# Optimization experiments

Hardware: AMD Instinct MI355X
Metric: run time of the kernel (lower is better)

The kernel has to match this reference:

```python
import jax, jax.numpy as jnp
import numpy as np

LSH_NUM_PROJS = 7
BLOCK_SIZE = 256      # key block size
SAMPLE_SIZE = 256
B, H, N, D = 1, 32, 8192, 128


def _gray_perm(num_projs):
    # AngularLSH._unit_hamming_distance_array: Gray-code bucket permutation
    a = np.array([0, 1], dtype=np.int32)
    for _ in range(num_projs - 1):
        a = np.concatenate([a, np.flip(a) + a.shape[0]])
    return jnp.asarray(a)


def _lsh_hash(x, proj_dir, perm):
    # x: [B,H,N,D], proj_dir: [D,R] -> bucket ids [B,H,N]
    bits = jnp.einsum('bhnd,dr->bhnr', x, proj_dir) > 0
    enc = 2 ** jnp.arange(proj_dir.shape[-1], dtype=jnp.int32)
    bin_ids = jnp.sum(bits.astype(jnp.int32) * enc, axis=-1)
    return perm[bin_ids]


def _attn_lse(q, k, v, scale, bias=None):
    # exact attention returning output and log-sum-exp of scaled scores
    s = jnp.einsum('...qd,...kd->...qk', q, k) * scale
    if bias is not None:
        s = s + bias
    m = jnp.max(s, axis=-1, keepdims=True)
    p = jnp.exp(s - m)
    denom = jnp.sum(p, axis=-1, keepdims=True)
    attn = jnp.einsum('...qk,...kd->...qd', p, v) / denom
    lse = m + jnp.log(denom)  # [..., q, 1]
    return attn, lse


def _take(x, idx):
    # gather along the sequence axis (dim 2); idx: [B,H,M]
    return jnp.take_along_axis(x, idx[..., None], axis=2)


def hyper_attention(q, k, v, proj_dir, sampled_set):
    b, h, n, d = q.shape
    scale = d ** -0.5
    perm = _gray_perm(LSH_NUM_PROJS)
    # 1) sortLSH: sort q and k by angular-LSH bucket (stable)
    q_idx = jnp.argsort(_lsh_hash(q, proj_dir, perm), axis=2)
    k_idx = jnp.argsort(_lsh_hash(k, proj_dir, perm), axis=2)
    q_idx_inv = jnp.argsort(q_idx, axis=2)
    q_s = _take(q, q_idx)
    k_s = _take(k, k_idx)
    v_s = _take(v, k_idx)
    nb = n // BLOCK_SIZE          # number of key blocks
    qbs = n // nb                 # query block size
    # block-diagonal exact attention in sorted order
    qb = q_s.reshape(b, h, nb, qbs, d)
    kb = k_s.reshape(b, h, nb, BLOCK_SIZE, d)
    vb = v_s.reshape(b, h, nb, BLOCK_SIZE, d)
    attn_blk, lse_blk = _attn_lse(qb, kb, vb, scale)
    attn_blk = attn_blk.reshape(b, h, n, d)
    lse_blk = lse_blk.reshape(b, h, n, 1)
    attn_blk = _take(attn_blk, q_idx_inv)
    lse_blk = _take(lse_blk, q_idx_inv)
    # 2) residual: uniform sampling of keys (indices into sorted key order)
    s_size = sampled_set.shape[-1]
    k_sub = _take(k_s, sampled_set)   # [B,H,S,D]
    v_sub = _take(v_s, sampled_set)
    # mask out samples falling in the query's own diagonal block
    same_block = (jnp.arange(n)[None, None, :, None] // qbs) == (sampled_set[:, :, None, :] // BLOCK_SIZE)
    bias = jnp.where(same_block, jnp.finfo(q.dtype).min, 0.0).astype(q.dtype)
    attn_res, lse_res = _attn_lse(q_s, k_sub, v_sub, scale, bias=bias)
    lse_res = lse_res + jnp.log(n / s_size)  # importance weight n_key/sample_size
    attn_res = _take(attn_res, q_idx_inv)
    lse_res = _take(lse_res, q_idx_inv)
    # 3) combine estimators: softmax-weighted average in log space
    lse = jnp.logaddexp(lse_blk, lse_res)
    return jnp.exp(lse_blk - lse) * attn_blk + jnp.exp(lse_res - lse) * attn_res


def setup_inputs() -> dict:
    key = jax.random.key(0)
    k1, k2, k3, k4, k5 = jax.random.split(key, 5)
    return {
        'queries': jax.random.normal(k1, (B, H, N, D), dtype=jnp.float32),
        'keys': jax.random.normal(k2, (B, H, N, D), dtype=jnp.float32),
        'vals': jax.random.normal(k3, (B, H, N, D), dtype=jnp.float32),
        'proj_dir': jax.random.normal(k4, (D, LSH_NUM_PROJS), dtype=jnp.float32),
        'sampled_set': jax.random.randint(k5, (B, H, SAMPLE_SIZE), 0, N),
    }


def reference(queries, keys, vals, proj_dir, sampled_set):
    return hyper_attention(queries, keys, vals, proj_dir, sampled_set)
```

## Files before the change

### kernel.cpp

```cpp
#include <hip/hip_runtime.h>
#include <hip/hip_bf16.h>
#include <math.h>

#define Hh 32
#define Nseq 8192
#define Dh 128
#define NBd 32
#define BLKSZ 256
#define SAMP 256
#define KVT 512
#define CHK 64
#define NCH 8
#define LOG32 3.4657359027997265f
#define SCALE 0.088388347648318447f
#define SKW 136

typedef float f32x4 __attribute__((ext_vector_type(4)));
typedef unsigned ui32x4 __attribute__((ext_vector_type(4)));
typedef __bf16 bf16x8 __attribute__((ext_vector_type(8)));

__device__ __forceinline__ f32x4 mfma16(bf16x8 a, bf16x8 b, f32x4 c) {
  return __builtin_amdgcn_mfma_f32_16x16x32_bf16(a, b, c, 0, 0, 0);
}

__device__ __forceinline__ bf16x8 cvt8(const float* __restrict__ p) {
  float4 a = ((const float4*)p)[0];
  float4 b = ((const float4*)p)[1];
  bf16x8 r;
  r[0] = (__bf16)a.x; r[1] = (__bf16)a.y; r[2] = (__bf16)a.z; r[3] = (__bf16)a.w;
  r[4] = (__bf16)b.x; r[5] = (__bf16)b.y; r[6] = (__bf16)b.z; r[7] = (__bf16)b.w;
  return r;
}

__device__ __forceinline__ bf16x8 cvt8v(float4 a, float4 b) {
  bf16x8 r;
  r[0] = (__bf16)a.x; r[1] = (__bf16)a.y; r[2] = (__bf16)a.z; r[3] = (__bf16)a.w;
  r[4] = (__bf16)b.x; r[5] = (__bf16)b.y; r[6] = (__bf16)b.z; r[7] = (__bf16)b.w;
  return r;
}

__device__ __forceinline__ unsigned packv(float a, float b) {
  __bf16 ba = (__bf16)a, bb = (__bf16)b;
  return ((unsigned)__builtin_bit_cast(unsigned short, bb) << 16) |
         (unsigned)__builtin_bit_cast(unsigned short, ba);
}

__device__ __forceinline__ unsigned pack2(float a, float b, float& ra, float& rb) {
  __bf16 ba = (__bf16)a, bb = (__bf16)b;
  ra = (float)ba; rb = (float)bb;
  return ((unsigned)__builtin_bit_cast(unsigned short, bb) << 16) |
         (unsigned)__builtin_bit_cast(unsigned short, ba);
}

__global__ __launch_bounds__(256) void lsh_hash_kernel(
    const float* __restrict__ q, const float* __restrict__ k,
    const float* __restrict__ proj, int* __restrict__ buckets) {
  int row = blockIdx.x * 256 + threadIdx.x;
  const float* x = ((row >> 18) ? k : q) + (size_t)(row & (Hh * Nseq - 1)) * Dh;
  double acc[7] = {0, 0, 0, 0, 0, 0, 0};
#pragma unroll 8
  for (int d0 = 0; d0 < Dh; d0 += 4) {
    float4 xv = *(const float4*)(x + d0);
    double x0 = (double)xv.x, x1 = (double)xv.y, x2 = (double)xv.z, x3 = (double)xv.w;
#pragma unroll
    for (int j = 0; j < 7; j++) {
      acc[j] = fma(x0, (double)proj[(d0 + 0) * 7 + j], acc[j]);
      acc[j] = fma(x1, (double)proj[(d0 + 1) * 7 + j], acc[j]);
      acc[j] = fma(x2, (double)proj[(d0 + 2) * 7 + j], acc[j]);
      acc[j] = fma(x3, (double)proj[(d0 + 3) * 7 + j], acc[j]);
    }
  }
  int bin = 0;
#pragma unroll
  for (int j = 0; j < 7; j++) bin |= (acc[j] > 0.0 ? 1 : 0) << j;
  buckets[row] = bin ^ (bin >> 1);
}

__global__ __launch_bounds__(64) void bucket_sort_kernel(
    const int* __restrict__ buckets, int* __restrict__ idx) {
  __shared__ unsigned hist[64][128];
  int t = threadIdx.x;
  int base = blockIdx.x * Nseq;
  for (int b = 0; b < 128; b++) hist[t][b] = 0;
  __syncthreads();
  for (int i = 0; i < 128; i++) {
    int b = buckets[base + t * 128 + i];
    hist[t][b]++;
  }
  __syncthreads();
  int b0 = 2 * t, b1 = 2 * t + 1;
  unsigned tot0 = 0, tot1 = 0;
  for (int tt = 0; tt < 64; tt++) { unsigned h = hist[tt][b0]; hist[tt][b0] = tot0; tot0 += h; }
  for (int tt = 0; tt < 64; tt++) { unsigned h = hist[tt][b1]; hist[tt][b1] = tot1; tot1 += h; }
  unsigned pair = tot0 + tot1;
  unsigned scan = pair;
  for (int s = 1; s < 64; s <<= 1) {
    unsigned u = __shfl_up(scan, s);
    if (t >= s) scan += u;
  }
  unsigned start0 = scan - pair;
  unsigned start1 = start0 + tot0;
  __syncthreads();
  for (int tt = 0; tt < 64; tt++) { hist[tt][b0] += start0; hist[tt][b1] += start1; }
  __syncthreads();
  for (int i = 0; i < 128; i++) {
    int gi = t * 128 + i;
    int b = buckets[base + gi];
    unsigned pos = hist[t][b]++;
    idx[base + pos] = gi;
  }
}

__global__ __launch_bounds__(512, 2) void hyper_attn_kernel(
    const float* __restrict__ q, const float* __restrict__ k, const float* __restrict__ v,
    const int* __restrict__ sampled, const int* __restrict__ q_idx,
    const int* __restrict__ k_idx, float* __restrict__ out) {
  __shared__ int s_orig[KVT];
  __shared__ __attribute__((aligned(16))) float s_add[KVT];
  __shared__ __attribute__((aligned(16))) __bf16 s_k[2][CHK][SKW];
  __shared__ __attribute__((aligned(16))) __bf16 s_vt[2][Dh][72];

  const int swz = ((blockIdx.x & 7) << 7) | (blockIdx.x >> 3);
  const int c = swz & 31, bh = swz >> 5;
  const int tid = threadIdx.x;
  const int w = tid >> 6, l = tid & 63;
  const int l4 = l >> 4, lm = l & 15;
  const int jk = tid >> 3, pk = tid & 7;
  const int kb = (tid & 31) * 2, dg = tid >> 5;

  {
    int jj = tid;
    if (jj < BLKSZ) {
      s_orig[jj] = k_idx[bh * Nseq + c * BLKSZ + jj];
      s_add[jj] = 0.0f;
    } else {
      int sp = sampled[bh * SAMP + (jj - BLKSZ)];
      s_orig[jj] = k_idx[bh * Nseq + sp];
      s_add[jj] = ((sp >> 8) == c) ? -1e38f : LOG32;
    }
  }

  bf16x8 qf[2][4];
  const int* qi = q_idx + bh * Nseq + c * BLKSZ + w * 32;
#pragma unroll
  for (int rt = 0; rt < 2; rt++) {
    int orig = qi[rt * 16 + lm];
    const float* qp = q + ((size_t)bh * Nseq + orig) * Dh + l4 * 8;
#pragma unroll
    for (int dc = 0; dc < 4; dc++) qf[rt][dc] = cvt8(qp + dc * 32);
  }

  f32x4 O[2][8];
  float mrow[2] = {-INFINITY, -INFINITY};
  float lsum[2] = {0.f, 0.f};
#pragma unroll
  for (int rt = 0; rt < 2; rt++)
#pragma unroll
    for (int dt = 0; dt < 8; dt++) { O[rt][dt][0]=0.f; O[rt][dt][1]=0.f; O[rt][dt][2]=0.f; O[rt][dt][3]=0.f; }

  __syncthreads();

  {
    int origk = s_orig[jk];
    const float* kp = k + ((size_t)bh * Nseq + origk) * Dh + pk * 16;
    *(bf16x8*)&s_k[0][jk][pk * 16]     = cvt8(kp);
    *(bf16x8*)&s_k[0][jk][pk * 16 + 8] = cvt8(kp + 8);
    int ra = s_orig[kb], rb = s_orig[kb + 1];
    const float4* va = (const float4*)(v + ((size_t)bh * Nseq + ra) * Dh + dg * 8);
    const float4* vb = (const float4*)(v + ((size_t)bh * Nseq + rb) * Dh + dg * 8);
    float4 A0 = va[0], A1 = va[1], B0 = vb[0], B1 = vb[1];
    float ta[8] = {A0.x,A0.y,A0.z,A0.w,A1.x,A1.y,A1.z,A1.w};
    float tb[8] = {B0.x,B0.y,B0.z,B0.w,B1.x,B1.y,B1.z,B1.w};
#pragma unroll
    for (int dd = 0; dd < 8; dd++)
      *(unsigned*)&s_vt[0][dg * 8 + dd][kb] = packv(ta[dd], tb[dd]);
  }
  __syncthreads();

  const int laneA = lm + 32 * (l4 & 1);
  const bool hi = (l4 >> 1) & 1;

  for (int ch = 0; ch < NCH; ch++) {
    const int cur = ch & 1;
    const bool pf = (ch + 1 < NCH);

    float4 kA, kB, kC, kD, vA0, vA1, vB0, vB1;
    if (pf) {
      int origk = s_orig[(ch + 1) * CHK + jk];
      const float4* kp = (const float4*)(k + ((size_t)bh * Nseq + origk) * Dh + pk * 16);
      kA = kp[0]; kB = kp[1]; kC = kp[2]; kD = kp[3];
      int ra = s_orig[(ch + 1) * CHK + kb], rb = s_orig[(ch + 1) * CHK + kb + 1];
      const float4* va = (const float4*)(v + ((size_t)bh * Nseq + ra) * Dh + dg * 8);
      const float4* vb = (const float4*)(v + ((size_t)bh * Nseq + rb) * Dh + dg * 8);
      vA0 = va[0]; vA1 = va[1]; vB0 = vb[0]; vB1 = vb[1];
    }
    __builtin_amdgcn_sched_barrier(0);

    float sc[2][4][4];
#pragma unroll
    for (int ct = 0; ct < 4; ct++) {
      f32x4 acc0, acc1;
      acc0[0]=0.f;acc0[1]=0.f;acc0[2]=0.f;acc0[3]=0.f;
      acc1[0]=0.f;acc1[1]=0.f;acc1[2]=0.f;acc1[3]=0.f;
#pragma unroll
      for (int dc = 0; dc < 4; dc++) {
        bf16x8 kf = *(const bf16x8*)&s_k[cur][ct * 16 + lm][dc * 32 + l4 * 8];
        acc0 = mfma16(kf, qf[0][dc], acc0);
        acc1 = mfma16(kf, qf[1][dc], acc1);
      }
      f32x4 addv = *(const f32x4*)&s_add[ch * CHK + ct * 16 + l4 * 4];
#pragma unroll
      for (int r = 0; r < 4; r++) {
        sc[0][ct][r] = acc0[r] * SCALE + addv[r];
        sc[1][ct][r] = acc1[r] * SCALE + addv[r];
      }
    }

    unsigned q01[2][4], q23[2][4];
#pragma unroll
    for (int rt = 0; rt < 2; rt++) {
      float mc = sc[rt][0][0];
#pragma unroll
      for (int ct = 0; ct < 4; ct++)
#pragma unroll
        for (int r = 0; r < 4; r++) mc = fmaxf(mc, sc[rt][ct][r]);
      mc = fmaxf(mc, __shfl_xor(mc, 16));
      mc = fmaxf(mc, __shfl_xor(mc, 32));
      float mn = fmaxf(mrow[rt], mc);
      float alpha = __expf(mrow[rt] - mn);
      mrow[rt] = mn;
      f32x4 aO;
#pragma unroll
      for (int r = 0; r < 4; r++) aO[r] = __shfl(alpha, l4 * 4 + r);
#pragma unroll
      for (int dt = 0; dt < 8; dt++) O[rt][dt] *= aO;
      float rsum = 0.f;
#pragma unroll
      for (int ct = 0; ct < 4; ct++) {
        float p0 = __expf(sc[rt][ct][0] - mn);
        float p1 = __expf(sc[rt][ct][1] - mn);
        float p2 = __expf(sc[rt][ct][2] - mn);
        float p3 = __expf(sc[rt][ct][3] - mn);
        float ra, rb, rc, rd;
        q01[rt][ct] = pack2(p0, p1, ra, rb);
        q23[rt][ct] = pack2(p2, p3, rc, rd);
        rsum += (ra + rb) + (rc + rd);
      }
      rsum += __shfl_xor(rsum, 16);
      rsum += __shfl_xor(rsum, 32);
      lsum[rt] = lsum[rt] * alpha + rsum;
    }

    if (pf) {
      *(bf16x8*)&s_k[cur ^ 1][jk][pk * 16]     = cvt8v(kA, kB);
      *(bf16x8*)&s_k[cur ^ 1][jk][pk * 16 + 8] = cvt8v(kC, kD);
      float ta[8] = {vA0.x,vA0.y,vA0.z,vA0.w,vA1.x,vA1.y,vA1.z,vA1.w};
      float tb[8] = {vB0.x,vB0.y,vB0.z,vB0.w,vB1.x,vB1.y,vB1.z,vB1.w};
#pragma unroll
      for (int dd = 0; dd < 8; dd++)
        *(unsigned*)&s_vt[cur ^ 1][dg * 8 + dd][kb] = packv(ta[dd], tb[dd]);
    }

#pragma unroll
    for (int kc = 0; kc < 2; kc++) {
      bf16x8 pa[2];
#pragma unroll
      for (int rt = 0; rt < 2; rt++) {
        unsigned a0 = __shfl((int)q01[rt][2 * kc],     laneA);
        unsigned b0 = __shfl((int)q01[rt][2 * kc + 1], laneA);
        unsigned a1 = __shfl((int)q23[rt][2 * kc],     laneA);
        unsigned b1 = __shfl((int)q23[rt][2 * kc + 1], laneA);
        unsigned a2 = __shfl((int)q01[rt][2 * kc],     laneA + 16);
        unsigned b2 = __shfl((int)q01[rt][2 * kc + 1], laneA + 16);
        unsigned a3 = __shfl((int)q23[rt][2 * kc],     laneA + 16);
        unsigned b3 = __shfl((int)q23[rt][2 * kc + 1], laneA + 16);
        ui32x4 pw;
        pw[0] = hi ? b0 : a0;
        pw[1] = hi ? b1 : a1;
        pw[2] = hi ? b2 : a2;
        pw[3] = hi ? b3 : a3;
        pa[rt] = __builtin_bit_cast(bf16x8, pw);
      }
#pragma unroll
      for (int dt = 0; dt < 8; dt++) {
        bf16x8 vb = *(const bf16x8*)&s_vt[cur][dt * 16 + lm][kc * 32 + l4 * 8];
        O[0][dt] = mfma16(pa[0], vb, O[0][dt]);
        O[1][dt] = mfma16(pa[1], vb, O[1][dt]);
      }
    }
    __syncthreads();
  }

#pragma unroll
  for (int rt = 0; rt < 2; rt++) {
    float inv = 1.0f / lsum[rt];
    f32x4 invr;
#pragma unroll
    for (int r = 0; r < 4; r++) invr[r] = __shfl(inv, l4 * 4 + r);
    int orow[4];
#pragma unroll
    for (int r = 0; r < 4; r++)
      orow[r] = q_idx[bh * Nseq + c * BLKSZ + w * 32 + rt * 16 + l4 * 4 + r];
#pragma unroll
    for (int r = 0; r < 4; r++) {
      float* op = out + ((size_t)bh * Nseq + orow[r]) * Dh + lm;
#pragma unroll
      for (int dt = 0; dt < 8; dt++) op[dt * 16] = O[rt][dt][r] * invr[r];
    }
  }
}

extern "C" void kernel_launch(void* const* d_in, const int* in_sizes, int n_in,
                              void* d_out, int out_size, void* d_ws, size_t ws_size,
                              hipStream_t stream) {
  const float* q    = (const float*)d_in[0];
  const float* k    = (const float*)d_in[1];
  const float* v    = (const float*)d_in[2];
  const float* proj = (const float*)d_in[3];
  const int* samp   = (const int*)d_in[4];
  float* out = (float*)d_out;

  int* buckets = (int*)d_ws;
  int* idx = buckets + 2 * Hh * Nseq;

  lsh_hash_kernel<<<(2 * Hh * Nseq) / 256, 256, 0, stream>>>(q, k, proj, buckets);
  bucket_sort_kernel<<<2 * Hh, 64, 0, stream>>>(buckets, idx);
  hyper_attn_kernel<<<NBd * Hh, 512, 0, stream>>>(
      q, k, v, samp, idx , idx + Hh * Nseq , out);
}
```

Baseline: 279.3 us.

## Split query block across two 256-thread workgroups with smaller KV chunks

Each 256-query block is now handled by two workgroups of 256 threads (128 queries each) rather than one of 512 threads. The grid doubles and launch bounds move to 4 workgroups per CU. KV chunks shrink from 64 to 32 keys, with a narrower transposed V buffer, to cut LDS use. The key index and the bias code are packed into one shared int array, which removes the separate float bias array. The aim is more occupancy and better load balance, at the cost of gathering each block's K/V twice and running twice as many chunk iterations, each with a barrier.

```diff
diff --git a/kernel.cpp b/kernel.cpp
--- a/kernel.cpp
+++ b/kernel.cpp
@@ -9,11 +9,12 @@
 #define BLKSZ 256
 #define SAMP 256
 #define KVT 512
-#define CHK 64
-#define NCH 8
+#define CHK 32
+#define NCH 16
 #define LOG32 3.4657359027997265f
 #define SCALE 0.088388347648318447f
 #define SKW 136
+#define SVW 40
 
 typedef float f32x4 __attribute__((ext_vector_type(4)));
 typedef unsigned ui32x4 __attribute__((ext_vector_type(4)));
@@ -50,6 +51,11 @@
   ra = (float)ba; rb = (float)bb;
   return ((unsigned)__builtin_bit_cast(unsigned short, bb) << 16) |
          (unsigned)__builtin_bit_cast(unsigned short, ba);
+}
+
+__device__ __forceinline__ float dec_add(int m) {
+  int cd = m >> 14;
+  return cd == 0 ? 0.0f : (cd == 1 ? LOG32 : -1e38f);
 }
 
 __global__ __launch_bounds__(256) void lsh_hash_kernel(
@@ -111,37 +117,40 @@
   }
 }
 
-__global__ __launch_bounds__(512, 2) void hyper_attn_kernel(
+__global__ __launch_bounds__(256, 4) void hyper_attn_kernel(
     const float* __restrict__ q, const float* __restrict__ k, const float* __restrict__ v,
     const int* __restrict__ sampled, const int* __restrict__ q_idx,
     const int* __restrict__ k_idx, float* __restrict__ out) {
-  __shared__ int s_orig[KVT];
-  __shared__ __attribute__((aligned(16))) float s_add[KVT];
+  __shared__ int s_meta[KVT];
   __shared__ __attribute__((aligned(16))) __bf16 s_k[2][CHK][SKW];
-  __shared__ __attribute__((aligned(16))) __bf16 s_vt[2][Dh][72];
-
-  const int swz = ((blockIdx.x & 7) << 7) | (blockIdx.x >> 3);
-  const int c = swz & 31, bh = swz >> 5;
+  __shared__ __attribute__((aligned(16))) __bf16 s_vt[2][Dh][SVW];
+
+  const int wg = ((blockIdx.x & 7) << 8) | (blockIdx.x >> 3);
+  const int bh = wg >> 6, c = (wg >> 1) & 31, hf = wg & 1;
   const int tid = threadIdx.x;
   const int w = tid >> 6, l = tid & 63;
   const int l4 = l >> 4, lm = l & 15;
   const int jk = tid >> 3, pk = tid & 7;
-  const int kb = (tid & 31) * 2, dg = tid >> 5;
+  const int kb = (tid & 15) * 2, dg = tid >> 4;
 
   {
-    int jj = tid;
-    if (jj < BLKSZ) {
-      s_orig[jj] = k_idx[bh * Nseq + c * BLKSZ + jj];
-      s_add[jj] = 0.0f;
-    } else {
-      int sp = sampled[bh * SAMP + (jj - BLKSZ)];
-      s_orig[jj] = k_idx[bh * Nseq + sp];
-      s_add[jj] = ((sp >> 8) == c) ? -1e38f : LOG32;
+#pragma unroll
+    for (int rep = 0; rep < 2; rep++) {
+      int jj = tid + rep * 256;
+      int m;
+      if (jj < BLKSZ) {
+        m = k_idx[bh * Nseq + c * BLKSZ + jj];
+      } else {
+        int sp = sampled[bh * SAMP + (jj - BLKSZ)];
+        int code = ((sp >> 8) == c) ? 2 : 1;
+        m = k_idx[bh * Nseq + sp] | (code << 14);
+      }
+      s_meta[jj] = m;
     }
   }
 
   bf16x8 qf[2][4];
-  const int* qi = q_idx + bh * Nseq + c * BLKSZ + w * 32;
+  const int* qi = q_idx + bh * Nseq + c * BLKSZ + hf * 128 + w * 32;
 #pragma unroll
   for (int rt = 0; rt < 2; rt++) {
     int orig = qi[rt * 16 + lm];
@@ -161,11 +170,11 @@
   __syncthreads();
 
   {
-    int origk = s_orig[jk];
-    const float* kp = k + ((size_t)bh * Nseq + origk) * Dh + pk * 16;
-    *(bf16x8*)&s_k[0][jk][pk * 16]     = cvt8(kp);
-    *(bf16x8*)&s_k[0][jk][pk * 16 + 8] = cvt8(kp + 8);
-    int ra = s_orig[kb], rb = s_orig[kb + 1];
+    int origk = s_meta[jk] & 8191;
+    const float4* kp = (const float4*)(k + ((size_t)bh * Nseq + origk) * Dh + pk * 16);
+    *(bf16x8*)&s_k[0][jk][pk * 16]     = cvt8v(kp[0], kp[1]);
+    *(bf16x8*)&s_k[0][jk][pk * 16 + 8] = cvt8v(kp[2], kp[3]);
+    int ra = s_meta[kb] & 8191, rb = s_meta[kb + 1] & 8191;
     const float4* va = (const float4*)(v + ((size_t)bh * Nseq + ra) * Dh + dg * 8);
     const float4* vb = (const float4*)(v + ((size_t)bh * Nseq + rb) * Dh + dg * 8);
     float4 A0 = va[0], A1 = va[1], B0 = vb[0], B1 = vb[1];
@@ -186,19 +195,20 @@
 
     float4 kA, kB, kC, kD, vA0, vA1, vB0, vB1;
     if (pf) {
-      int origk = s_orig[(ch + 1) * CHK + jk];
+      int origk = s_meta[(ch + 1) * CHK + jk] & 8191;
       const float4* kp = (const float4*)(k + ((size_t)bh * Nseq + origk) * Dh + pk * 16);
       kA = kp[0]; kB = kp[1]; kC = kp[2]; kD = kp[3];
-      int ra = s_orig[(ch + 1) * CHK + kb], rb = s_orig[(ch + 1) * CHK + kb + 1];
+      int ra = s_meta[(ch + 1) * CHK + kb] & 8191;
+      int rb = s_meta[(ch + 1) * CHK + kb + 1] & 8191;
       const float4* va = (const float4*)(v + ((size_t)bh * Nseq + ra) * Dh + dg * 8);
       const float4* vb = (const float4*)(v + ((size_t)bh * Nseq + rb) * Dh + dg * 8);
       vA0 = va[0]; vA1 = va[1]; vB0 = vb[0]; vB1 = vb[1];
     }
     __builtin_amdgcn_sched_barrier(0);
 
-    float sc[2][4][4];
-#pragma unroll
-    for (int ct = 0; ct < 4; ct++) {
+    float sc[2][2][4];
+#pragma unroll
+    for (int ct = 0; ct < 2; ct++) {
       f32x4 acc0, acc1;
       acc0[0]=0.f;acc0[1]=0.f;acc0[2]=0.f;acc0[3]=0.f;
       acc1[0]=0.f;acc1[1]=0.f;acc1[2]=0.f;acc1[3]=0.f;
@@ -208,20 +218,21 @@
         acc0 = mfma16(kf, qf[0][dc], acc0);
         acc1 = mfma16(kf, qf[1][dc], acc1);
       }
-      f32x4 addv = *(const f32x4*)&s_add[ch * CHK + ct * 16 + l4 * 4];
+      ui32x4 mv = *(const ui32x4*)&s_meta[ch * CHK + ct * 16 + l4 * 4];
 #pragma unroll
       for (int r = 0; r < 4; r++) {
-        sc[0][ct][r] = acc0[r] * SCALE + addv[r];
-        sc[1][ct][r] = acc1[r] * SCALE + addv[r];
-      }
-    }
-
-    unsigned q01[2][4], q23[2][4];
+        float add = dec_add((int)mv[r]);
+        sc[0][ct][r] = acc0[r] * SCALE + add;
+        sc[1][ct][r] = acc1[r] * SCALE + add;
+      }
+    }
+
+    unsigned q01[2][2], q23[2][2];
 #pragma unroll
     for (int rt = 0; rt < 2; rt++) {
       float mc = sc[rt][0][0];
 #pragma unroll
-      for (int ct = 0; ct < 4; ct++)
+      for (int ct = 0; ct < 2; ct++)
 #pragma unroll
         for (int r = 0; r < 4; r++) mc = fmaxf(mc, sc[rt][ct][r]);
       mc = fmaxf(mc, __shfl_xor(mc, 16));
@@ -236,7 +247,7 @@
       for (int dt = 0; dt < 8; dt++) O[rt][dt] *= aO;
       float rsum = 0.f;
 #pragma unroll
-      for (int ct = 0; ct < 4; ct++) {
+      for (int ct = 0; ct < 2; ct++) {
         float p0 = __expf(sc[rt][ct][0] - mn);
         float p1 = __expf(sc[rt][ct][1] - mn);
         float p2 = __expf(sc[rt][ct][2] - mn);
@@ -261,19 +272,18 @@
         *(unsigned*)&s_vt[cur ^ 1][dg * 8 + dd][kb] = packv(ta[dd], tb[dd]);
     }
 
-#pragma unroll
-    for (int kc = 0; kc < 2; kc++) {
+    {
       bf16x8 pa[2];
 #pragma unroll
       for (int rt = 0; rt < 2; rt++) {
-        unsigned a0 = __shfl((int)q01[rt][2 * kc],     laneA);
-        unsigned b0 = __shfl((int)q01[rt][2 * kc + 1], laneA);
-        unsigned a1 = __shfl((int)q23[rt][2 * kc],     laneA);
-        unsigned b1 = __shfl((int)q23[rt][2 * kc + 1], laneA);
-        unsigned a2 = __shfl((int)q01[rt][2 * kc],     laneA + 16);
-        unsigned b2 = __shfl((int)q01[rt][2 * kc + 1], laneA + 16);
-        unsigned a3 = __shfl((int)q23[rt][2 * kc],     laneA + 16);
-        unsigned b3 = __shfl((int)q23[rt][2 * kc + 1], laneA + 16);
+        unsigned a0 = __shfl((int)q01[rt][0], laneA);
+        unsigned b0 = __shfl((int)q01[rt][1], laneA);
+        unsigned a1 = __shfl((int)q23[rt][0], laneA);
+        unsigned b1 = __shfl((int)q23[rt][1], laneA);
+        unsigned a2 = __shfl((int)q01[rt][0], laneA + 16);
+        unsigned b2 = __shfl((int)q01[rt][1], laneA + 16);
+        unsigned a3 = __shfl((int)q23[rt][0], laneA + 16);
+        unsigned b3 = __shfl((int)q23[rt][1], laneA + 16);
         ui32x4 pw;
         pw[0] = hi ? b0 : a0;
         pw[1] = hi ? b1 : a1;
@@ -283,7 +293,7 @@
       }
 #pragma unroll
       for (int dt = 0; dt < 8; dt++) {
-        bf16x8 vb = *(const bf16x8*)&s_vt[cur][dt * 16 + lm][kc * 32 + l4 * 8];
+        bf16x8 vb = *(const bf16x8*)&s_vt[cur][dt * 16 + lm][l4 * 8];
         O[0][dt] = mfma16(pa[0], vb, O[0][dt]);
         O[1][dt] = mfma16(pa[1], vb, O[1][dt]);
       }
@@ -300,7 +310,7 @@
     int orow[4];
 #pragma unroll
     for (int r = 0; r < 4; r++)
-      orow[r] = q_idx[bh * Nseq + c * BLKSZ + w * 32 + rt * 16 + l4 * 4 + r];
+      orow[r] = q_idx[bh * Nseq + c * BLKSZ + hf * 128 + w * 32 + rt * 16 + l4 * 4 + r];
 #pragma unroll
     for (int r = 0; r < 4; r++) {
       float* op = out + ((size_t)bh * Nseq + orow[r]) * Dh + lm;
@@ -325,6 +335,6 @@
 
   lsh_hash_kernel<<<(2 * Hh * Nseq) / 256, 256, 0, stream>>>(q, k, proj, buckets);
   bucket_sort_kernel<<<2 * Hh, 64, 0, stream>>>(buckets, idx);
-  hyper_attn_kernel<<<NBd * Hh, 512, 0, stream>>>(
+  hyper_attn_kernel<<<2 * NBd * Hh, 256, 0, stream>>>(
       q, k, v, samp, idx , idx + Hh * Nseq , out);
 }
```

After: 731.2 us. 162% more time.
